# Optimization experiments

Hardware: AMD Instinct MI355X
Metric: run time of the kernel (lower is better)

Reference implementation:

```python
import jax, jax.numpy as jnp
import numpy as np

B, L, D_IN, D_MODEL, H = 8, 1024, 256, 512, 8
D_HEAD = D_MODEL // H


def setup_inputs() -> dict:
    key = jax.random.key(0)
    ks = jax.random.split(key, 12)
    queries = jax.random.normal(ks[0], (B, L, D_IN), dtype=jnp.float32)
    keys_ = jax.random.normal(ks[1], (B, L, D_IN), dtype=jnp.float32)
    values = jax.random.normal(ks[2], (B, L, D_IN), dtype=jnp.float32)
    attention_mask = jnp.ones((B, L), dtype=jnp.int32)
    # binary symmetric-ish adjacency (sparse molecular graph style)
    adjacency_matrix = (jax.random.uniform(ks[3], (B, L, L)) < 0.05).astype(jnp.float32)
    distance_matrix = jax.random.uniform(ks[4], (B, L, L), dtype=jnp.float32) * 10.0
    s = 1.0 / np.sqrt(D_IN)
    W_q = jax.random.normal(ks[5], (D_MODEL, D_IN), dtype=jnp.float32) * s
    W_k = jax.random.normal(ks[6], (D_MODEL, D_IN), dtype=jnp.float32) * s
    W_v = jax.random.normal(ks[7], (D_MODEL, D_IN), dtype=jnp.float32) * s
    W_o = jax.random.normal(ks[8], (D_MODEL, D_MODEL), dtype=jnp.float32) / np.sqrt(D_MODEL)
    lambda_a = jax.random.normal(ks[9], (H,), dtype=jnp.float32) * 0.1
    lambda_d = jax.random.normal(ks[10], (H,), dtype=jnp.float32) * 0.1
    return {"queries": queries, "keys": keys_, "values": values,
            "attention_mask": attention_mask, "adjacency_matrix": adjacency_matrix,
            "distance_matrix": distance_matrix, "W_q": W_q, "W_k": W_k,
            "W_v": W_v, "W_o": W_o, "lambda_a": lambda_a, "lambda_d": lambda_d}


def _split_heads(x):
    # (b, l, d_model) -> (b, h, l, d_head)
    b, l, _ = x.shape
    return x.reshape(b, l, H, D_HEAD).transpose(0, 2, 1, 3)


def reference(queries, keys, values, attention_mask, adjacency_matrix,
              distance_matrix, W_q, W_k, W_v, W_o, lambda_a, lambda_d):
    Q = _split_heads(queries @ W_q.T)   # (b,h,l,d)
    K = _split_heads(keys @ W_k.T)
    V = _split_heads(values @ W_v.T)
    scores = jnp.einsum("bhqd,bhkd->bhqk", Q, K) / jnp.sqrt(jnp.asarray(D_HEAD, Q.dtype))
    # MSRSA: per-head learned scalars inject graph structure into the scores
    scores = (scores
              + lambda_a[None, :, None, None] * adjacency_matrix[:, None, :, :]
              + lambda_d[None, :, None, None] * distance_matrix[:, None, :, :])
    mask = attention_mask[:, None, None, :] > 0  # (b,1,1,l) key mask
    scores = jnp.where(mask, scores, jnp.asarray(-1e9, scores.dtype))
    attn_weight = jax.nn.softmax(scores, axis=-1)  # (b,h,l,l)
    out = jnp.einsum("bhqk,bhkd->bhqd", attn_weight, V)
    out = out.transpose(0, 2, 1, 3).reshape(queries.shape[0], queries.shape[1], D_MODEL)
    return out @ W_o.T
```

## Files before the change

kernel.cpp:

```cpp
#include <hip/hip_runtime.h>
#include <hip/hip_fp16.h>

#define BB 8
#define LL 1024
#define DIN 256
#define DM 512
#define HH 8
#define DH 64

typedef __attribute__((ext_vector_type(8))) short bf16x8;
typedef __attribute__((ext_vector_type(4))) float f32x4;

__device__ __forceinline__ unsigned short f2bf(float f) {
  union { float f; unsigned u; } c; c.f = f;
  unsigned u = c.u;
  return (unsigned short)((u + 0x7fffu + ((u >> 16) & 1u)) >> 16);
}

#if defined(__has_builtin)
#if __has_builtin(__builtin_amdgcn_cvt_pk_bf16_f32)
#define HAS_PK_BF16 1
#endif
#endif

#ifdef HAS_PK_BF16
typedef __bf16 bf2 __attribute__((ext_vector_type(2)));
__device__ __forceinline__ unsigned pk2(float lo, float hi) {
  union { bf2 v; unsigned u; } c;
  c.v = __builtin_amdgcn_cvt_pk_bf16_f32(lo, hi);
  return c.u;
}
#else
__device__ __forceinline__ unsigned pk2(float lo, float hi) {
  return ((unsigned)f2bf(hi) << 16) | f2bf(lo);
}
#endif

__device__ __forceinline__ unsigned pkh(float a, float d) {
  return (unsigned)__half_as_ushort(__float2half_rn(a)) |
         ((unsigned)__half_as_ushort(__float2half_rn(d)) << 16);
}

__device__ __forceinline__ void async_copy16(void* lds, const void* g) {
  __builtin_amdgcn_global_load_lds(
      (const __attribute__((address_space(1))) unsigned*)g,
      (__attribute__((address_space(3))) unsigned*)lds, 16, 0, 0);
}

__global__ __launch_bounds__(256) void prep(
    const float* __restrict__ qin, const float* __restrict__ kin,
    const float* __restrict__ vin,
    const float* __restrict__ wq, const float* __restrict__ wk,
    const float* __restrict__ wv, const float* __restrict__ wo,
    const int* __restrict__ msk,
    const float* __restrict__ adj, const float* __restrict__ dis,
    unsigned short* __restrict__ xq, unsigned short* __restrict__ xk,
    unsigned short* __restrict__ xv,
    unsigned short* __restrict__ wqb, unsigned short* __restrict__ wkb,
    unsigned short* __restrict__ wvb, unsigned short* __restrict__ wob,
    float* __restrict__ mad, unsigned* __restrict__ bp)
{
  int t = blockIdx.x * 256 + threadIdx.x;
  const int XS = 524288, WS = 32768;
  if (t < 3 * XS) {
    int seg = t >> 19, off = t & (XS - 1);
    const float* s = (seg == 0) ? qin : (seg == 1) ? kin : vin;
    unsigned short* d = (seg == 0) ? xq : (seg == 1) ? xk : xv;
    float4 f = ((const float4*)s)[off];
    uint2 o = { pk2(f.x, f.y), pk2(f.z, f.w) };
    ((uint2*)d)[off] = o;
    return;
  }
  t -= 3 * XS;
  if (t < 3 * WS) {
    int seg = t >> 15, off = t & (WS - 1);
    const float* s = (seg == 0) ? wq : (seg == 1) ? wk : wv;
    unsigned short* d = (seg == 0) ? wqb : (seg == 1) ? wkb : wvb;
    float4 f = ((const float4*)s)[off];
    uint2 o = { pk2(f.x, f.y), pk2(f.z, f.w) };
    ((uint2*)d)[off] = o;
    return;
  }
  t -= 3 * WS;
  if (t < 65536) {
    float4 f = ((const float4*)wo)[t];
    uint2 o = { pk2(f.x, f.y), pk2(f.z, f.w) };
    ((uint2*)wob)[t] = o;
    return;
  }
  t -= 65536;
  if (t < 2048) {
    int4 m = ((const int4*)msk)[t];
    float4 f = { m.x ? 0.0f : -30000.0f, m.y ? 0.0f : -30000.0f,
                 m.z ? 0.0f : -30000.0f, m.w ? 0.0f : -30000.0f };
    ((float4*)mad)[t] = f;
    return;
  }
  t -= 2048;
  float4 a4 = ((const float4*)adj)[t];
  float4 d4 = ((const float4*)dis)[t];
  uint4 o = { pkh(a4.x, d4.x), pkh(a4.y, d4.y), pkh(a4.z, d4.z), pkh(a4.w, d4.w) };
  ((uint4*)bp)[t] = o;
}

__global__ __launch_bounds__(256) void qkv_proj(
    const unsigned short* __restrict__ xq, const unsigned short* __restrict__ xk,
    const unsigned short* __restrict__ xv,
    const unsigned short* __restrict__ wqb, const unsigned short* __restrict__ wkb,
    const unsigned short* __restrict__ wvb,
    unsigned short* __restrict__ qb, unsigned short* __restrict__ kb,
    unsigned short* __restrict__ vt)
{
  const int t = blockIdx.z;
  const unsigned short* __restrict__ X = (t == 0) ? xq : (t == 1) ? xk : xv;
  const unsigned short* __restrict__ W = (t == 0) ? wqb : (t == 1) ? wkb : wvb;
  const int m0 = blockIdx.y * 128;
  const int h  = blockIdx.x;
  __shared__ unsigned short As[128 * 40];
  __shared__ unsigned short Bs[64 * 40];
  const int tid = threadIdx.x;
  const int wid = tid >> 6;
  const int lane = tid & 63;
  const int lo = lane & 15;
  const int quad = lane >> 4;

  f32x4 acc[2][4];
#pragma unroll
  for (int mi = 0; mi < 2; ++mi)
#pragma unroll
    for (int ni = 0; ni < 4; ++ni) acc[mi][ni] = (f32x4)0.0f;

  for (int kk = 0; kk < DIN; kk += 32) {
#pragma unroll
    for (int i = 0; i < 2; ++i) {
      int id = i * 256 + tid;
      int row = id >> 2, ch = id & 3;
      *(uint4*)&As[row * 40 + ch * 8] =
          *(const uint4*)&X[(size_t)(m0 + row) * DIN + kk + ch * 8];
    }
    {
      int row = tid >> 2, ch = tid & 3;
      *(uint4*)&Bs[row * 40 + ch * 8] =
          *(const uint4*)&W[(size_t)(h * 64 + row) * DIN + kk + ch * 8];
    }
    __syncthreads();
    bf16x8 a[2], bfr[4];
#pragma unroll
    for (int mi = 0; mi < 2; ++mi)
      a[mi] = *(const bf16x8*)&As[(wid * 32 + mi * 16 + lo) * 40 + quad * 8];
#pragma unroll
    for (int ni = 0; ni < 4; ++ni)
      bfr[ni] = *(const bf16x8*)&Bs[(ni * 16 + lo) * 40 + quad * 8];
#pragma unroll
    for (int mi = 0; mi < 2; ++mi)
#pragma unroll
      for (int ni = 0; ni < 4; ++ni)
        acc[mi][ni] = __builtin_amdgcn_mfma_f32_16x16x32_bf16(
            a[mi], bfr[ni], acc[mi][ni], 0, 0, 0);
    __syncthreads();
  }

  const int b = m0 >> 10;
  const int lbase0 = (m0 & 1023) + wid * 32;
  if (t < 2) {
    unsigned short* dstp = (t == 0) ? qb : kb;
#pragma unroll
    for (int mi = 0; mi < 2; ++mi)
#pragma unroll
      for (int ni = 0; ni < 4; ++ni) {
        int d = ni * 16 + lo;
#pragma unroll
        for (int r = 0; r < 4; ++r) {
          int lb = lbase0 + mi * 16 + quad * 4 + r;
          dstp[((size_t)(b * HH + h) * LL + lb) * DH + d] = f2bf(acc[mi][ni][r]);
        }
      }
  } else {
#pragma unroll
    for (int mi = 0; mi < 2; ++mi)
#pragma unroll
      for (int ni = 0; ni < 4; ++ni) {
        int d = ni * 16 + lo;
        int lb = lbase0 + mi * 16 + quad * 4;
        uint2 o = { pk2(acc[mi][ni][0], acc[mi][ni][1]),
                    pk2(acc[mi][ni][2], acc[mi][ni][3]) };
        *(uint2*)&vt[((size_t)(b * HH + h) * DH + d) * LL + lb] = o;
      }
  }
}

__global__ __launch_bounds__(256) void attn(
    const unsigned short* __restrict__ qb, const unsigned short* __restrict__ kb,
    const unsigned short* __restrict__ vt,
    const float* __restrict__ mad, const unsigned* __restrict__ bp,
    const float* __restrict__ la_, const float* __restrict__ ld_,
    unsigned short* __restrict__ ao)
{
  const int bi = blockIdx.x;
  const int b  = bi & 7;
  const int hg = (bi >> 3) & 3;
  const int q0 = (bi >> 5) * 32;
  const int tid = threadIdx.x;
  const int wid = tid >> 6;
  const int lane = tid & 63;
  const int lo = lane & 15;
  const int quad = lane >> 4;
  const int h  = hg * 2 + (wid & 1);
  const int kh = wid >> 1;
  const int bh = b * HH + h;

  __shared__ __align__(16) char arena[34816];
  unsigned short* kbufw = (unsigned short*)(arena) + wid * 2048;
  unsigned*       bbuf  = (unsigned*)(arena + 16384);
  unsigned short* pbufw = (unsigned short*)(arena + 24576) + wid * 1280;
  float*          mgbuf = (float*)arena;

  const float LOG2E = 1.44269504f;
  const float la2 = la_[h] * LOG2E, ld2 = ld_[h] * LOG2E;
  const float sc2 = 0.125f * LOG2E;

  const unsigned short* qp = qb + ((size_t)bh * LL + q0) * DH;
  bf16x8 qB[2][2];
#pragma unroll
  for (int nj = 0; nj < 2; ++nj)
#pragma unroll
    for (int ki = 0; ki < 2; ++ki)
      qB[nj][ki] = *(const bf16x8*)&qp[(nj * 16 + lo) * DH + ki * 32 + quad * 8];

  const unsigned short* kp = kb + (size_t)bh * LL * DH;
  const unsigned short* vp = vt + (size_t)bh * DH * LL;
  const unsigned* bpp = bp + ((size_t)b * LL + q0) * LL;
  const float* mp = mad + b * LL;

  f32x4 o[4][2];
  float rs[2] = {0.0f, 0.0f};
#pragma unroll
  for (int md = 0; md < 4; ++md)
#pragma unroll
    for (int nj = 0; nj < 2; ++nj) o[md][nj] = (f32x4)0.0f;

  const int kbeg = kh * (LL / 2);
  const int r8 = lane >> 3, p8 = lane & 7;

  for (int jt = 0; jt < 16; ++jt) {
    const int k0 = kbeg + jt * 32;

    {
      const unsigned short* kg = kp + (size_t)k0 * DH;
#pragma unroll
      for (int j = 0; j < 4; ++j)
        async_copy16(kbufw + j * 512,
                     kg + (j * 8 + r8) * 64 + ((p8 ^ r8) * 8));
      if ((wid & 1) == 0) {
        const int khs = wid >> 1;
        const unsigned* bg = bpp + khs * (LL / 2) + jt * 32;
        unsigned* bb = bbuf + khs * 1024;
#pragma unroll
        for (int j = 0; j < 4; ++j)
          async_copy16(bb + j * 256,
                       bg + (size_t)(j * 8 + r8) * LL + ((p8 ^ r8) * 4));
      }
    }
    bf16x8 vA[4];
#pragma unroll
    for (int md = 0; md < 4; ++md)
      vA[md] = *(const bf16x8*)&vp[(md * 16 + lo) * LL + k0 + quad * 8];
    f32x4 msv[2];
#pragma unroll
    for (int mi = 0; mi < 2; ++mi)
      msv[mi] = *(const f32x4*)&mp[k0 + mi * 16 + quad * 4];

    __syncthreads();

    bf16x8 kA[2][2];
#pragma unroll
    for (int mi = 0; mi < 2; ++mi)
#pragma unroll
      for (int ki = 0; ki < 2; ++ki)
        kA[mi][ki] = *(const bf16x8*)&kbufw[(mi * 16 + lo) * 64 +
                                            (((ki * 4 + quad) ^ (lo & 7)) * 8)];
    f32x4 s[2][2];
#pragma unroll
    for (int mi = 0; mi < 2; ++mi)
#pragma unroll
      for (int nj = 0; nj < 2; ++nj) s[mi][nj] = (f32x4)0.0f;
#pragma unroll
    for (int ki = 0; ki < 2; ++ki)
#pragma unroll
      for (int mi = 0; mi < 2; ++mi)
#pragma unroll
        for (int nj = 0; nj < 2; ++nj)
          s[mi][nj] = __builtin_amdgcn_mfma_f32_16x16x32_bf16(
              kA[mi][ki], qB[nj][ki], s[mi][nj], 0, 0, 0);

#pragma unroll
    for (int mi = 0; mi < 2; ++mi)
#pragma unroll
      for (int nj = 0; nj < 2; ++nj) {
        uint4 u = *(const uint4*)&bbuf[kh * 1024 + (nj * 16 + lo) * 32 +
                                       (((mi * 4 + quad) ^ (lo & 7)) * 4)];
        float p[4];
#pragma unroll
        for (int r = 0; r < 4; ++r) {
          union { unsigned v; __half2 hh; } c; c.v = u[r];
          float tt = fmaf(__high2float(c.hh), ld2, msv[mi][r]);
          tt = fmaf(__low2float(c.hh), la2, tt);
          p[r] = __builtin_amdgcn_exp2f(fmaf(s[mi][nj][r], sc2, tt));
        }
        rs[nj] += (p[0] + p[1]) + (p[2] + p[3]);
        uint2 w = { pk2(p[0], p[1]), pk2(p[2], p[3]) };
        *(uint2*)&pbufw[(nj * 16 + lo) * 40 + mi * 16 + quad * 4] = w;
      }

    asm volatile("s_waitcnt lgkmcnt(0)" ::: "memory");

    bf16x8 pB[2];
#pragma unroll
    for (int nj = 0; nj < 2; ++nj)
      pB[nj] = *(const bf16x8*)&pbufw[(nj * 16 + lo) * 40 + quad * 8];

#pragma unroll
    for (int md = 0; md < 4; ++md)
#pragma unroll
      for (int nj = 0; nj < 2; ++nj)
        o[md][nj] = __builtin_amdgcn_mfma_f32_16x16x32_bf16(
            vA[md], pB[nj], o[md][nj], 0, 0, 0);

    __syncthreads();
  }

  const int hs = wid & 1;
  if (kh == 1) {
#pragma unroll
    for (int md = 0; md < 4; ++md)
#pragma unroll
      for (int nj = 0; nj < 2; ++nj)
#pragma unroll
        for (int r = 0; r < 4; ++r)
          mgbuf[hs * 2176 + ((md * 2 + nj) * 4 + r) * 64 + lane] = o[md][nj][r];
    mgbuf[hs * 2176 + 32 * 64 + lane] = rs[0];
    mgbuf[hs * 2176 + 33 * 64 + lane] = rs[1];
  }
  __syncthreads();
  if (kh == 0) {
#pragma unroll
    for (int md = 0; md < 4; ++md)
#pragma unroll
      for (int nj = 0; nj < 2; ++nj)
#pragma unroll
        for (int r = 0; r < 4; ++r)
          o[md][nj][r] += mgbuf[hs * 2176 + ((md * 2 + nj) * 4 + r) * 64 + lane];
    rs[0] += mgbuf[hs * 2176 + 32 * 64 + lane];
    rs[1] += mgbuf[hs * 2176 + 33 * 64 + lane];
    float inv[2];
#pragma unroll
    for (int nj = 0; nj < 2; ++nj) {
      rs[nj] += __shfl_xor(rs[nj], 16);
      rs[nj] += __shfl_xor(rs[nj], 32);
      inv[nj] = __builtin_amdgcn_rcpf(rs[nj]);
    }
#pragma unroll
    for (int md = 0; md < 4; ++md)
#pragma unroll
      for (int nj = 0; nj < 2; ++nj) {
        int l = q0 + nj * 16 + lo;
        uint2 st = { pk2(o[md][nj][0] * inv[nj], o[md][nj][1] * inv[nj]),
                     pk2(o[md][nj][2] * inv[nj], o[md][nj][3] * inv[nj]) };
        *(uint2*)&ao[((size_t)b * LL + l) * DM + h * DH + md * 16 + quad * 4] = st;
      }
  }
}

__global__ __launch_bounds__(256) void oproj(
    const unsigned short* __restrict__ ao, const unsigned short* __restrict__ wob,
    float* __restrict__ out)
{
  const int m0 = blockIdx.y * 128;
  const int n0 = blockIdx.x * 64;
  __shared__ unsigned short As[128 * 40];
  __shared__ unsigned short Bs[64 * 40];
  const int tid = threadIdx.x;
  const int wid = tid >> 6;
  const int lane = tid & 63;
  const int lo = lane & 15;
  const int quad = lane >> 4;

  f32x4 acc[2][4];
#pragma unroll
  for (int mi = 0; mi < 2; ++mi)
#pragma unroll
    for (int ni = 0; ni < 4; ++ni) acc[mi][ni] = (f32x4)0.0f;

  for (int kk = 0; kk < DM; kk += 32) {
#pragma unroll
    for (int i = 0; i < 2; ++i) {
      int id = i * 256 + tid;
      int row = id >> 2, ch = id & 3;
      *(uint4*)&As[row * 40 + ch * 8] =
          *(const uint4*)&ao[(size_t)(m0 + row) * DM + kk + ch * 8];
    }
    {
      int row = tid >> 2, ch = tid & 3;
      *(uint4*)&Bs[row * 40 + ch * 8] =
          *(const uint4*)&wob[(size_t)(n0 + row) * DM + kk + ch * 8];
    }
    __syncthreads();
    bf16x8 a[2], bfr[4];
#pragma unroll
    for (int mi = 0; mi < 2; ++mi)
      a[mi] = *(const bf16x8*)&As[(wid * 32 + mi * 16 + lo) * 40 + quad * 8];
#pragma unroll
    for (int ni = 0; ni < 4; ++ni)
      bfr[ni] = *(const bf16x8*)&Bs[(ni * 16 + lo) * 40 + quad * 8];
#pragma unroll
    for (int mi = 0; mi < 2; ++mi)
#pragma unroll
      for (int ni = 0; ni < 4; ++ni)
        acc[mi][ni] = __builtin_amdgcn_mfma_f32_16x16x32_bf16(
            a[mi], bfr[ni], acc[mi][ni], 0, 0, 0);
    __syncthreads();
  }

#pragma unroll
  for (int mi = 0; mi < 2; ++mi)
#pragma unroll
    for (int ni = 0; ni < 4; ++ni)
#pragma unroll
      for (int r = 0; r < 4; ++r)
        out[(size_t)(m0 + wid * 32 + mi * 16 + quad * 4 + r) * DM +
            n0 + ni * 16 + lo] = acc[mi][ni][r];
}

extern "C" void kernel_launch(void* const* d_in, const int* in_sizes, int n_in,
                              void* d_out, int out_size, void* d_ws, size_t ws_size,
                              hipStream_t stream) {
  const float* qin = (const float*)d_in[0];
  const float* kin = (const float*)d_in[1];
  const float* vin = (const float*)d_in[2];
  const int*   msk = (const int*)d_in[3];
  const float* adj = (const float*)d_in[4];
  const float* dis = (const float*)d_in[5];
  const float* wq  = (const float*)d_in[6];
  const float* wk  = (const float*)d_in[7];
  const float* wv  = (const float*)d_in[8];
  const float* wo  = (const float*)d_in[9];
  const float* la  = (const float*)d_in[10];
  const float* ld  = (const float*)d_in[11];
  float* out = (float*)d_out;

  const size_t tensb = (size_t)BB * HH * LL * DH;
  const size_t xsz   = (size_t)BB * LL * DIN;
  unsigned short* qb  = (unsigned short*)d_ws;
  unsigned short* kb  = qb + tensb;
  unsigned short* vt  = kb + tensb;
  unsigned short* ao  = vt + tensb;
  unsigned short* xq  = ao;
  unsigned short* xk  = ao + xsz;
  unsigned short* xv  = ao + tensb;
  unsigned short* wqb = xv + xsz;
  unsigned short* wkb = wqb + (size_t)DM * DIN;
  unsigned short* wvb = wkb + (size_t)DM * DIN;
  unsigned short* wob = wvb + (size_t)DM * DIN;
  float*          mdd = (float*)(wob + (size_t)DM * DM);
  unsigned*       bpk = (unsigned*)(mdd + (size_t)BB * LL);

  prep<<<dim3(14984), 256, 0, stream>>>(qin, kin, vin, wq, wk, wv, wo, msk,
                                        adj, dis,
                                        xq, xk, xv, wqb, wkb, wvb, wob, mdd, bpk);
  qkv_proj<<<dim3(8, 64, 3), 256, 0, stream>>>(xq, xk, xv, wqb, wkb, wvb, qb, kb, vt);
  attn<<<dim3(1024), 256, 0, stream>>>(qb, kb, vt, mdd, bpk, la, ld, ao);
  oproj<<<dim3(8, 64), 256, 0, stream>>>(ao, wob, out);
}
```

Before: 245.6 us.

## Double-buffer LDS tiles with async copies in projection and attention kernels

Converts the QKV projection, output projection and attention kernels to a two-stage LDS ping-pong. The next K/bias (or X/W) tile is issued with async global-to-LDS copies while the current tile is consumed, so each iteration no longer waits for its own loads. GEMM tiles switch from padded rows to an XOR-swizzled layout to avoid bank conflicts. LDS use grows (the attention arena goes from about 34KB to 58KB), which may lower occupancy, and correctness depends on barrier placement around buffer reuse.

```diff
diff --git a/kernel.cpp b/kernel.cpp
--- a/kernel.cpp
+++ b/kernel.cpp
@@ -116,8 +116,7 @@
   const unsigned short* __restrict__ W = (t == 0) ? wqb : (t == 1) ? wkb : wvb;
   const int m0 = blockIdx.y * 128;
   const int h  = blockIdx.x;
-  __shared__ unsigned short As[128 * 40];
-  __shared__ unsigned short Bs[64 * 40];
+  __shared__ __align__(16) char arena[24576];
   const int tid = threadIdx.x;
   const int wid = tid >> 6;
   const int lane = tid & 63;
@@ -130,27 +129,48 @@
 #pragma unroll
     for (int ni = 0; ni < 4; ++ni) acc[mi][ni] = (f32x4)0.0f;
 
-  for (int kk = 0; kk < DIN; kk += 32) {
-#pragma unroll
-    for (int i = 0; i < 2; ++i) {
-      int id = i * 256 + tid;
-      int row = id >> 2, ch = id & 3;
-      *(uint4*)&As[row * 40 + ch * 8] =
-          *(const uint4*)&X[(size_t)(m0 + row) * DIN + kk + ch * 8];
-    }
-    {
-      int row = tid >> 2, ch = tid & 3;
-      *(uint4*)&Bs[row * 40 + ch * 8] =
-          *(const uint4*)&W[(size_t)(h * 64 + row) * DIN + kk + ch * 8];
-    }
-    __syncthreads();
+#pragma unroll
+  for (int j = 0; j < 2; ++j) {
+    int id = j * 256 + tid, r = id >> 2, c = id & 3;
+    async_copy16(arena + j * 4096 + wid * 1024,
+                 X + (size_t)(m0 + r) * DIN + ((c ^ (r & 3)) * 8));
+  }
+  {
+    int id = tid, r = id >> 2, c = id & 3;
+    async_copy16(arena + 16384 + wid * 1024,
+                 W + (size_t)(h * 64 + r) * DIN + ((c ^ (r & 3)) * 8));
+  }
+  __syncthreads();
+
+  for (int it = 0; it < 8; ++it) {
+    const int p = it & 1;
+    if (it < 7) {
+      const int kk = (it + 1) * 32, q = 1 - p;
+#pragma unroll
+      for (int j = 0; j < 2; ++j) {
+        int id = j * 256 + tid, r = id >> 2, c = id & 3;
+        async_copy16(arena + q * 8192 + j * 4096 + wid * 1024,
+                     X + (size_t)(m0 + r) * DIN + kk + ((c ^ (r & 3)) * 8));
+      }
+      {
+        int id = tid, r = id >> 2, c = id & 3;
+        async_copy16(arena + 16384 + q * 4096 + wid * 1024,
+                     W + (size_t)(h * 64 + r) * DIN + kk + ((c ^ (r & 3)) * 8));
+      }
+    }
+    const unsigned short* Ab = (const unsigned short*)(arena + p * 8192);
+    const unsigned short* Bb = (const unsigned short*)(arena + 16384 + p * 4096);
     bf16x8 a[2], bfr[4];
 #pragma unroll
-    for (int mi = 0; mi < 2; ++mi)
-      a[mi] = *(const bf16x8*)&As[(wid * 32 + mi * 16 + lo) * 40 + quad * 8];
-#pragma unroll
-    for (int ni = 0; ni < 4; ++ni)
-      bfr[ni] = *(const bf16x8*)&Bs[(ni * 16 + lo) * 40 + quad * 8];
+    for (int mi = 0; mi < 2; ++mi) {
+      int R = wid * 32 + mi * 16 + lo;
+      a[mi] = *(const bf16x8*)&Ab[R * 32 + ((quad ^ (R & 3)) * 8)];
+    }
+#pragma unroll
+    for (int ni = 0; ni < 4; ++ni) {
+      int N = ni * 16 + lo;
+      bfr[ni] = *(const bf16x8*)&Bb[N * 32 + ((quad ^ (N & 3)) * 8)];
+    }
 #pragma unroll
     for (int mi = 0; mi < 2; ++mi)
 #pragma unroll
@@ -209,10 +229,8 @@
   const int kh = wid >> 1;
   const int bh = b * HH + h;
 
-  __shared__ __align__(16) char arena[34816];
-  unsigned short* kbufw = (unsigned short*)(arena) + wid * 2048;
-  unsigned*       bbuf  = (unsigned*)(arena + 16384);
-  unsigned short* pbufw = (unsigned short*)(arena + 24576) + wid * 1280;
+  __shared__ __align__(16) char arena[59392];
+  unsigned short* pbufw = (unsigned short*)(arena + 49152) + wid * 1280;
   float*          mgbuf = (float*)arena;
 
   const float LOG2E = 1.44269504f;
@@ -242,25 +260,44 @@
   const int kbeg = kh * (LL / 2);
   const int r8 = lane >> 3, p8 = lane & 7;
 
+  {
+    const unsigned short* kg = kp + (size_t)kbeg * DH;
+#pragma unroll
+    for (int j = 0; j < 4; ++j)
+      async_copy16(arena + wid * 4096 + j * 1024,
+                   kg + (j * 8 + r8) * 64 + ((p8 ^ r8) * 8));
+    if ((wid & 1) == 0) {
+      const int khs = wid >> 1;
+      const unsigned* bg = bpp + khs * (LL / 2);
+#pragma unroll
+      for (int j = 0; j < 4; ++j)
+        async_copy16(arena + 32768 + khs * 4096 + j * 1024,
+                     bg + (size_t)(j * 8 + r8) * LL + ((p8 ^ r8) * 4));
+    }
+  }
+  __syncthreads();
+
   for (int jt = 0; jt < 16; ++jt) {
+    const int p = jt & 1;
     const int k0 = kbeg + jt * 32;
 
-    {
-      const unsigned short* kg = kp + (size_t)k0 * DH;
+    if (jt < 15) {
+      const int kn = k0 + 32, q = 1 - p;
+      const unsigned short* kg = kp + (size_t)kn * DH;
 #pragma unroll
       for (int j = 0; j < 4; ++j)
-        async_copy16(kbufw + j * 512,
+        async_copy16(arena + q * 16384 + wid * 4096 + j * 1024,
                      kg + (j * 8 + r8) * 64 + ((p8 ^ r8) * 8));
       if ((wid & 1) == 0) {
         const int khs = wid >> 1;
-        const unsigned* bg = bpp + khs * (LL / 2) + jt * 32;
-        unsigned* bb = bbuf + khs * 1024;
+        const unsigned* bg = bpp + khs * (LL / 2) + (jt + 1) * 32;
 #pragma unroll
         for (int j = 0; j < 4; ++j)
-          async_copy16(bb + j * 256,
+          async_copy16(arena + 32768 + q * 8192 + khs * 4096 + j * 1024,
                        bg + (size_t)(j * 8 + r8) * LL + ((p8 ^ r8) * 4));
       }
     }
+
     bf16x8 vA[4];
 #pragma unroll
     for (int md = 0; md < 4; ++md)
@@ -270,15 +307,16 @@
     for (int mi = 0; mi < 2; ++mi)
       msv[mi] = *(const f32x4*)&mp[k0 + mi * 16 + quad * 4];
 
-    __syncthreads();
+    const unsigned short* kbf = (const unsigned short*)(arena + p * 16384) + wid * 2048;
+    const unsigned* bbf = (const unsigned*)(arena + 32768 + p * 8192) + kh * 1024;
 
     bf16x8 kA[2][2];
 #pragma unroll
     for (int mi = 0; mi < 2; ++mi)
 #pragma unroll
       for (int ki = 0; ki < 2; ++ki)
-        kA[mi][ki] = *(const bf16x8*)&kbufw[(mi * 16 + lo) * 64 +
-                                            (((ki * 4 + quad) ^ (lo & 7)) * 8)];
+        kA[mi][ki] = *(const bf16x8*)&kbf[(mi * 16 + lo) * 64 +
+                                          (((ki * 4 + quad) ^ (lo & 7)) * 8)];
     f32x4 s[2][2];
 #pragma unroll
     for (int mi = 0; mi < 2; ++mi)
@@ -297,18 +335,18 @@
     for (int mi = 0; mi < 2; ++mi)
 #pragma unroll
       for (int nj = 0; nj < 2; ++nj) {
-        uint4 u = *(const uint4*)&bbuf[kh * 1024 + (nj * 16 + lo) * 32 +
-                                       (((mi * 4 + quad) ^ (lo & 7)) * 4)];
-        float p[4];
+        uint4 u = *(const uint4*)&bbf[(nj * 16 + lo) * 32 +
+                                      (((mi * 4 + quad) ^ (lo & 7)) * 4)];
+        float p4[4];
 #pragma unroll
         for (int r = 0; r < 4; ++r) {
           union { unsigned v; __half2 hh; } c; c.v = u[r];
           float tt = fmaf(__high2float(c.hh), ld2, msv[mi][r]);
           tt = fmaf(__low2float(c.hh), la2, tt);
-          p[r] = __builtin_amdgcn_exp2f(fmaf(s[mi][nj][r], sc2, tt));
+          p4[r] = __builtin_amdgcn_exp2f(fmaf(s[mi][nj][r], sc2, tt));
         }
-        rs[nj] += (p[0] + p[1]) + (p[2] + p[3]);
-        uint2 w = { pk2(p[0], p[1]), pk2(p[2], p[3]) };
+        rs[nj] += (p4[0] + p4[1]) + (p4[2] + p4[3]);
+        uint2 w = { pk2(p4[0], p4[1]), pk2(p4[2], p4[3]) };
         *(uint2*)&pbufw[(nj * 16 + lo) * 40 + mi * 16 + quad * 4] = w;
       }
 
@@ -377,8 +415,7 @@
 {
   const int m0 = blockIdx.y * 128;
   const int n0 = blockIdx.x * 64;
-  __shared__ unsigned short As[128 * 40];
-  __shared__ unsigned short Bs[64 * 40];
+  __shared__ __align__(16) char arena[24576];
   const int tid = threadIdx.x;
   const int wid = tid >> 6;
   const int lane = tid & 63;
@@ -391,27 +428,48 @@
 #pragma unroll
     for (int ni = 0; ni < 4; ++ni) acc[mi][ni] = (f32x4)0.0f;
 
-  for (int kk = 0; kk < DM; kk += 32) {
-#pragma unroll
-    for (int i = 0; i < 2; ++i) {
-      int id = i * 256 + tid;
-      int row = id >> 2, ch = id & 3;
-      *(uint4*)&As[row * 40 + ch * 8] =
-          *(const uint4*)&ao[(size_t)(m0 + row) * DM + kk + ch * 8];
-    }
-    {
-      int row = tid >> 2, ch = tid & 3;
-      *(uint4*)&Bs[row * 40 + ch * 8] =
-          *(const uint4*)&wob[(size_t)(n0 + row) * DM + kk + ch * 8];
-    }
-    __syncthreads();
+#pragma unroll
+  for (int j = 0; j < 2; ++j) {
+    int id = j * 256 + tid, r = id >> 2, c = id & 3;
+    async_copy16(arena + j * 4096 + wid * 1024,
+                 ao + (size_t)(m0 + r) * DM + ((c ^ (r & 3)) * 8));
+  }
+  {
+    int id = tid, r = id >> 2, c = id & 3;
+    async_copy16(arena + 16384 + wid * 1024,
+                 wob + (size_t)(n0 + r) * DM + ((c ^ (r & 3)) * 8));
+  }
+  __syncthreads();
+
+  for (int it = 0; it < 16; ++it) {
+    const int p = it & 1;
+    if (it < 15) {
+      const int kk = (it + 1) * 32, q = 1 - p;
+#pragma unroll
+      for (int j = 0; j < 2; ++j) {
+        int id = j * 256 + tid, r = id >> 2, c = id & 3;
+        async_copy16(arena + q * 8192 + j * 4096 + wid * 1024,
+                     ao + (size_t)(m0 + r) * DM + kk + ((c ^ (r & 3)) * 8));
+      }
+      {
+        int id = tid, r = id >> 2, c = id & 3;
+        async_copy16(arena + 16384 + q * 4096 + wid * 1024,
+                     wob + (size_t)(n0 + r) * DM + kk + ((c ^ (r & 3)) * 8));
+      }
+    }
+    const unsigned short* Ab = (const unsigned short*)(arena + p * 8192);
+    const unsigned short* Bb = (const unsigned short*)(arena + 16384 + p * 4096);
     bf16x8 a[2], bfr[4];
 #pragma unroll
-    for (int mi = 0; mi < 2; ++mi)
-      a[mi] = *(const bf16x8*)&As[(wid * 32 + mi * 16 + lo) * 40 + quad * 8];
-#pragma unroll
-    for (int ni = 0; ni < 4; ++ni)
-      bfr[ni] = *(const bf16x8*)&Bs[(ni * 16 + lo) * 40 + quad * 8];
+    for (int mi = 0; mi < 2; ++mi) {
+      int R = wid * 32 + mi * 16 + lo;
+      a[mi] = *(const bf16x8*)&Ab[R * 32 + ((quad ^ (R & 3)) * 8)];
+    }
+#pragma unroll
+    for (int ni = 0; ni < 4; ++ni) {
+      int N = ni * 16 + lo;
+      bfr[ni] = *(const bf16x8*)&Bb[N * 32 + ((quad ^ (N & 3)) * 8)];
+    }
 #pragma unroll
     for (int mi = 0; mi < 2; ++mi)
 #pragma unroll
```

New measurement: 233.9 us. 4.8% less time.
